# Performance work log

Hardware: AMD Instinct MI355X
Metric: run time of the kernel (lower is better)

The kernel has to match this reference:

```python
import jax, jax.numpy as jnp
import numpy as np

D_MODEL = 1024
NUM_HEADS = 16
DEPTH = D_MODEL // NUM_HEADS
B, S = 2, 2048
NEG = -1e9


def setup_inputs() -> dict:
    key = jax.random.key(0)
    ks = jax.random.split(key, 12)
    sc = 1.0 / np.sqrt(D_MODEL)
    inp = {
        "query": jax.random.normal(ks[0], (B, S, D_MODEL), jnp.float32),
        "key_in": jax.random.normal(ks[1], (B, S, D_MODEL), jnp.float32),
        "value": jax.random.normal(ks[2], (B, S, D_MODEL), jnp.float32),
        # causal mask: 1.0 where attention is disallowed (upper triangle)
        "mask": (1.0 - jnp.tril(jnp.ones((S, S), jnp.float32)))[None, None, :, :],
        "wq": jax.random.normal(ks[3], (D_MODEL, D_MODEL), jnp.float32) * sc,
        "bq": jnp.zeros((D_MODEL,), jnp.float32),
        "wk": jax.random.normal(ks[4], (D_MODEL, D_MODEL), jnp.float32) * sc,
        "bk": jnp.zeros((D_MODEL,), jnp.float32),
        "wv": jax.random.normal(ks[5], (D_MODEL, D_MODEL), jnp.float32) * sc,
        "bv": jnp.zeros((D_MODEL,), jnp.float32),
        "wo": jax.random.normal(ks[6], (D_MODEL, D_MODEL), jnp.float32) * sc,
        "bo": jnp.zeros((D_MODEL,), jnp.float32),
    }
    return inp


def _split_heads(x):
    # [B,S,D] -> [B,H,S,depth]
    b, s, _ = x.shape
    return x.reshape(b, s, NUM_HEADS, DEPTH).transpose(0, 2, 1, 3)


def reference(query, key_in, value, mask, wq, bq, wk, bk, wv, bv, wo, bo):
    q = _split_heads(query @ wq + bq)
    k = _split_heads(key_in @ wk + bk)
    v = _split_heads(value @ wv + bv)
    scale = 1.0 / jnp.sqrt(jnp.asarray(DEPTH, jnp.float32))
    logits = jnp.einsum("bhqd,bhkd->bhqk", q, k) * scale + mask * NEG
    attn = jax.nn.softmax(logits, axis=-1)
    out = jnp.einsum("bhqk,bhkd->bhqd", attn, v)  # [B,H,S,depth]
    out = out.transpose(0, 2, 1, 3).reshape(query.shape[0], -1, D_MODEL)
    return out @ wo + bo
```

## Files before the change

kernel.cpp:

```cpp
#include <hip/hip_runtime.h>
#include <hip/hip_bf16.h>
#include <cstdint>
#include <cstddef>

#define D_MODEL 1024
#define NHEADS  16
#define DEPTH   64
#define BATCH   2
#define SEQ     2048
#define M_TOT   (BATCH*SEQ)
#define QK_SCALE 0.18033688011112042f

typedef __attribute__((ext_vector_type(8)))  __bf16 bf16x8;
typedef __attribute__((ext_vector_type(4)))  float  f32x4;
typedef __attribute__((ext_vector_type(16))) float  f32x16;

__device__ inline unsigned short f2bf(float f){
  unsigned u = __float_as_uint(f);
  u += 0x7FFFu + ((u>>16)&1u);
  return (unsigned short)(u>>16);
}
__device__ inline unsigned cvtpk(float lo, float hi){
  unsigned r;
  asm("v_cvt_pk_bf16_f32 %0, %1, %2" : "=v"(r) : "v"(lo), "v"(hi));
  return r;
}
__device__ inline float fexp2(float x){
  float r;
  asm("v_exp_f32 %0, %1" : "=v"(r) : "v"(x));
  return r;
}
__device__ inline int bswap23(int x){
  return (x & ~12) | ((x & 4) << 1) | ((x & 8) >> 1);
}

#define AS1(p) ((__attribute__((address_space(1))) void*)(p))
#define AS3(p) ((__attribute__((address_space(3))) void*)(p))

__global__ void tcvt4(const float* __restrict__ w0, const float* __restrict__ w1,
                      const float* __restrict__ w2, const float* __restrict__ w3,
                      unsigned short* o0, unsigned short* o1,
                      unsigned short* o2, unsigned short* o3){
  const float* W = blockIdx.z==0 ? w0 : blockIdx.z==1 ? w1 : blockIdx.z==2 ? w2 : w3;
  unsigned short* Wt = blockIdx.z==0 ? o0 : blockIdx.z==1 ? o1 : blockIdx.z==2 ? o2 : o3;
  const bool perm = (blockIdx.z == 3);
  __shared__ float t[32][33];
  int bx = blockIdx.x*32, by = blockIdx.y*32;
  for (int j = threadIdx.y; j < 32; j += 8)
    t[j][threadIdx.x] = W[(size_t)(by+j)*D_MODEL + bx + threadIdx.x];
  __syncthreads();
  for (int j = threadIdx.y; j < 32; j += 8){
    int col = by + threadIdx.x;
    if (perm) col = bswap23(col);
    Wt[(size_t)(bx+j)*D_MODEL + col] = f2bf(t[threadIdx.x][j]);
  }
}

#define BK 32
#define GK 1024
#define NSTEP (GK/BK)

__global__ __launch_bounds__(256,4) void gemm_qkv(
    const float* __restrict__ Xfq, const float* __restrict__ Xfk,
    const float* __restrict__ Xfv,
    const unsigned short* __restrict__ Wq, const unsigned short* __restrict__ Wk,
    const unsigned short* __restrict__ Wv,
    const float* __restrict__ bq, const float* __restrict__ bk, const float* __restrict__ bv,
    unsigned short* Qh, unsigned short* Kh, unsigned short* Vth)
{
  __shared__ __align__(16) short As[2][64*BK];
  __shared__ __align__(16) short Bs[2][128*BK];
  const int z = blockIdx.z;
  const float* Af          = z==0 ? Xfq : z==1 ? Xfk : Xfv;
  const unsigned short* Bt = z==0 ? Wq  : z==1 ? Wk  : Wv;
  const float* bias        = z==0 ? bq  : z==1 ? bk  : bv;

  const int tid = threadIdx.x, lane = tid & 63, wave = tid >> 6;
  const int m0 = blockIdx.x*64, n0 = blockIdx.y*128;
  const int wm = wave >> 1, wn = wave & 1;

  f32x4 acc[2][4];
  #pragma unroll
  for (int i=0;i<2;i++)
    #pragma unroll
    for (int j=0;j<4;j++)
      acc[i][j] = (f32x4){0.f,0.f,0.f,0.f};

  const char* Afb   = (const char*)Af + (size_t)m0*GK*4;
  const char* Bbase = (const char*)Bt + (size_t)n0*GK*2;
  const int arow = tid >> 2;
  const int acb  = (tid & 3) * 32;

  float4 a0lo, a0hi, a1lo, a1hi;

#define LOADA0(k0) { \
    const char* p_ = Afb + (size_t)arow*(GK*4) + (size_t)(k0)*4 + acb; \
    a0lo = *(const float4*)p_; a0hi = *(const float4*)(p_ + 16); }
#define LOADA1(k0) { \
    const char* p_ = Afb + (size_t)arow*(GK*4) + (size_t)(k0)*4 + acb; \
    a1lo = *(const float4*)p_; a1hi = *(const float4*)(p_ + 16); }

#define ISSUEB(t, BUF) \
  _Pragma("unroll") \
  for (int c=0;c<2;c++) \
    __builtin_amdgcn_global_load_lds( \
      AS1(Bbase + (size_t)(c*64 + arow)*(GK*2) + (size_t)(t)*64 + (tid&3)*16), \
      AS3((char*)&Bs[BUF][0] + c*4096 + tid*16), 16, 0, 0);

#define CVTWR0() { \
    uint4 pk_; \
    pk_.x = cvtpk(a0lo.x, a0lo.y); pk_.y = cvtpk(a0lo.z, a0lo.w); \
    pk_.z = cvtpk(a0hi.x, a0hi.y); pk_.w = cvtpk(a0hi.z, a0hi.w); \
    *(uint4*)((char*)&As[0][0] + tid*16) = pk_; }
#define CVTWR1() { \
    uint4 pk_; \
    pk_.x = cvtpk(a1lo.x, a1lo.y); pk_.y = cvtpk(a1lo.z, a1lo.w); \
    pk_.z = cvtpk(a1hi.x, a1hi.y); pk_.w = cvtpk(a1hi.z, a1hi.w); \
    *(uint4*)((char*)&As[1][0] + tid*16) = pk_; }

#define MFMA_PHASE(BUF) { \
    bf16x8 af_[2], bv_[4]; \
    _Pragma("unroll") \
    for (int i=0;i<2;i++) \
      af_[i] = *(const bf16x8*)((const char*)&As[BUF][0] + (wm*32+i*16+(lane&15))*64 + (lane>>4)*16); \
    _Pragma("unroll") \
    for (int j=0;j<4;j++) \
      bv_[j] = *(const bf16x8*)((const char*)&Bs[BUF][0] + (wn*64+j*16+(lane&15))*64 + (lane>>4)*16); \
    _Pragma("unroll") \
    for (int i=0;i<2;i++) \
      _Pragma("unroll") \
      for (int j=0;j<4;j++) \
        acc[i][j] = __builtin_amdgcn_mfma_f32_16x16x32_bf16(af_[i], bv_[j], acc[i][j], 0,0,0); }

  LOADA0(0)
  ISSUEB(0, 0)
  LOADA1(BK)
  CVTWR0()

  #pragma unroll 1
  for (int t = 0; t < NSTEP; t += 2){
    __syncthreads();
    if (t+1 < NSTEP) ISSUEB(t+1, 1)
    if (t+2 < NSTEP) LOADA0((t+2)*BK)
    if (t+1 < NSTEP) CVTWR1()
    MFMA_PHASE(0)
    __syncthreads();
    if (t+2 < NSTEP) ISSUEB(t+2, 0)
    if (t+3 < NSTEP) LOADA1((t+3)*BK)
    if (t+2 < NSTEP) CVTWR0()
    MFMA_PHASE(1)
  }

  #pragma unroll
  for (int i=0;i<2;i++)
    #pragma unroll
    for (int j=0;j<4;j++)
      #pragma unroll
      for (int r=0;r<4;r++){
        int gr = m0 + wm*32 + i*16 + (lane>>4)*4 + r;
        int gc = n0 + wn*64 + j*16 + (lane&15);
        float v = acc[i][j][r] + bias[gc];
        int b = gr>>11, s = gr&2047, h = gc>>6, d = gc&63;
        if (z == 0){
          v *= QK_SCALE;
          Qh[(((size_t)(b*NHEADS+h))*SEQ + s)*DEPTH + d] = f2bf(v);
        } else if (z == 1){
          Kh[(((size_t)(b*NHEADS+h))*SEQ + s)*DEPTH + d] = f2bf(v);
        } else {
          int sp = bswap23(s);
          Vth[(((size_t)(b*NHEADS+h))*DEPTH + d)*SEQ + sp] = f2bf(v);
        }
      }
#undef LOADA0
#undef LOADA1
#undef ISSUEB
#undef CVTWR0
#undef CVTWR1
#undef MFMA_PHASE
}

__global__ __launch_bounds__(256,4) void gemm_out(
    const unsigned short* __restrict__ A,
    const unsigned short* __restrict__ Bt,
    const float* __restrict__ bias,
    float* __restrict__ Cout)
{
  __shared__ __align__(16) short As[2][64*BK];
  __shared__ __align__(16) short Bs[2][64*BK];
  const int tid = threadIdx.x, lane = tid & 63, wave = tid >> 6;
  const int m0 = blockIdx.x*64, n0 = blockIdx.y*64;
  const int wm = wave >> 1, wn = wave & 1;

  f32x4 acc[2][2];
  #pragma unroll
  for (int i=0;i<2;i++)
    #pragma unroll
    for (int j=0;j<2;j++)
      acc[i][j] = (f32x4){0.f,0.f,0.f,0.f};

  const char* Abase = (const char*)A + (size_t)m0*GK*2;
  const char* Bbase = (const char*)Bt + (size_t)n0*GK*2;

  auto STAGE = [&](int t){
    __builtin_amdgcn_global_load_lds(
      AS1(Abase + (size_t)(tid>>2)*(GK*2) + (size_t)t*64 + (tid&3)*16),
      AS3((char*)&As[t&1][0] + tid*16), 16, 0, 0);
    __builtin_amdgcn_global_load_lds(
      AS1(Bbase + (size_t)(tid>>2)*(GK*2) + (size_t)t*64 + (tid&3)*16),
      AS3((char*)&Bs[t&1][0] + tid*16), 16, 0, 0);
  };

  STAGE(0);
  #pragma unroll 1
  for (int t = 0; t < NSTEP; ++t){
    __syncthreads();
    if (t+1 < NSTEP) STAGE(t+1);
    bf16x8 af[2], bfv[2];
    #pragma unroll
    for (int i=0;i<2;i++)
      af[i] = *(const bf16x8*)((const char*)&As[t&1][0] + (wm*32 + i*16 + (lane&15))*64 + (lane>>4)*16);
    #pragma unroll
    for (int j=0;j<2;j++)
      bfv[j] = *(const bf16x8*)((const char*)&Bs[t&1][0] + (wn*32 + j*16 + (lane&15))*64 + (lane>>4)*16);
    #pragma unroll
    for (int i=0;i<2;i++)
      #pragma unroll
      for (int j=0;j<2;j++)
        acc[i][j] = __builtin_amdgcn_mfma_f32_16x16x32_bf16(af[i], bfv[j], acc[i][j], 0,0,0);
  }

  #pragma unroll
  for (int i=0;i<2;i++)
    #pragma unroll
    for (int j=0;j<2;j++)
      #pragma unroll
      for (int r=0;r<4;r++){
        int gr = m0 + wm*32 + i*16 + (lane>>4)*4 + r;
        int gc = n0 + wn*32 + j*16 + (lane&15);
        Cout[(size_t)gr*D_MODEL + gc] = acc[i][j][r] + bias[gc];
      }
}

__global__ __launch_bounds__(512,4) void attn_fwd(
  const unsigned short* __restrict__ Qh,
  const unsigned short* __restrict__ Kh,
  const unsigned short* __restrict__ Vt,
  unsigned short* __restrict__ AO)
{
  __shared__ __align__(16) short Ks[2][4096];
  __shared__ __align__(16) short Vs[2][4096];
  __shared__ float cbS[2][128];

  const int tid = threadIdx.x, lane = tid & 63, w = tid >> 6;
  const int h = lane >> 5, ql = lane & 31;
  const int qh = w & 1, kh = (w >> 1) & 1, tl = w >> 2;
  const int pj = blockIdx.x, bh = blockIdx.y;
  const size_t hb = (size_t)bh * SEQ * DEPTH;
  const char* Kb = (const char*)(Kh + hb);
  const char* Vb = (const char*)(Vt + hb);
  const unsigned short* Qb = Qh + hb;
  const int bb = bh >> 4, hd = bh & 15;
  const int swz = (ql & 7) << 4;

  auto STAGE = [&](int buf, int t){
    const int kv0 = t*64;
    #pragma unroll
    for (int i=0;i<2;i++){
      int c = (w&3)*2 + i;
      int x = c*1024 + lane*16;
      int row = x >> 7;
      int cb = (x & 127) ^ ((row&7)<<4);
      if (w < 4)
        __builtin_amdgcn_global_load_lds(
          AS1(Kb + (size_t)(kv0+row)*128 + cb),
          AS3((char*)&Ks[buf][0] + c*1024), 16, 0, 0);
      else
        __builtin_amdgcn_global_load_lds(
          AS1(Vb + ((size_t)row*SEQ + kv0)*2 + cb),
          AS3((char*)&Vs[buf][0] + c*1024), 16, 0, 0);
    }
  };

  const int jtw = tl ? pj : (31 - pj);
  const int Q0 = jtw*64 + qh*32;
  const int qmax = Q0 + 31;
  const int Tblock = 32 - pj;

  bf16x8 qreg[4];
  {
    const unsigned short* qp = Qb + (size_t)(Q0 + ql)*DEPTH + h*8;
    #pragma unroll
    for (int c=0;c<4;c++) qreg[c] = *(const bf16x8*)(qp + c*16);
  }

  f32x16 oacc[2];
  #pragma unroll
  for (int dh=0;dh<2;dh++)
    #pragma unroll
    for (int r=0;r<16;r++) oacc[dh][r] = 0.f;
  float s = 0.f;

  STAGE(0, 0);
  __syncthreads();
  int cur = 0;

  #pragma unroll 1
  for (int t = 0; t < Tblock; ++t){
    if (t+1 < Tblock) STAGE(cur^1, t+1);
    const int kvb = t*64 + kh*32;

    if (kvb <= qmax){
      f32x16 sa;
      #pragma unroll
      for (int r=0;r<16;r++) sa[r] = -16.0f;
      #pragma unroll
      for (int c=0;c<4;c++){
        bf16x8 kf = *(const bf16x8*)((const char*)&Ks[cur][0]
                      + (kh*32 + ql)*128 + ((32*c + 16*h) ^ swz));
        sa = __builtin_amdgcn_mfma_f32_32x32x16_bf16(kf, qreg[c], sa, 0,0,0);
      }

      if (kvb + 31 > Q0){
        const int qg = Q0 + ql - kvb;
        #pragma unroll
        for (int r=0;r<16;r++){
          int pos = (r&3) + 8*(r>>2) + 4*h;
          sa[r] = (pos > qg) ? -1e9f : sa[r];
        }
      }

      float s0=0.f, s1=0.f, s2=0.f, s3=0.f;
      #pragma unroll
      for (int r=0;r<16;r++){
        float p = fexp2(sa[r]);
        sa[r] = p;
        if ((r&3)==0) s0 += p; else if ((r&3)==1) s1 += p;
        else if ((r&3)==2) s2 += p; else s3 += p;
      }
      s += (s0+s1)+(s2+s3);

      bf16x8 pw[2];
      #pragma unroll
      for (int ks=0;ks<2;ks++){
        const int mm = 8*ks;
        union { unsigned u[4]; bf16x8 v; } pk;
        pk.u[0] = cvtpk(sa[mm+0], sa[mm+1]);
        pk.u[1] = cvtpk(sa[mm+2], sa[mm+3]);
        pk.u[2] = cvtpk(sa[mm+4], sa[mm+5]);
        pk.u[3] = cvtpk(sa[mm+6], sa[mm+7]);
        pw[ks] = pk.v;
      }

      #pragma unroll
      for (int ks=0;ks<2;ks++){
        #pragma unroll
        for (int dh=0;dh<2;dh++){
          bf16x8 vf = *(const bf16x8*)((const char*)&Vs[cur][0]
                        + (dh*32 + ql)*128 + ((kh*64 + ks*32 + 16*h) ^ swz));
          oacc[dh] = __builtin_amdgcn_mfma_f32_32x32x16_bf16(vf, pw[ks], oacc[dh], 0,0,0);
        }
      }
    }

    __syncthreads();
    cur ^= 1;
  }

  float* cbO  = (tl == 0) ? (float*)&Ks[0][0] : (float*)&Vs[0][0];
  float* cbSp = &cbS[tl][0];
  if (kh == 1){
    #pragma unroll
    for (int dh=0;dh<2;dh++)
      #pragma unroll
      for (int r=0;r<16;r++)
        cbO[(dh*16+r)*128 + qh*64 + lane] = oacc[dh][r];
    cbSp[qh*64 + lane] = s;
  }
  __syncthreads();
  if (kh == 0){
    #pragma unroll
    for (int dh=0;dh<2;dh++)
      #pragma unroll
      for (int r=0;r<16;r++)
        oacc[dh][r] += cbO[(dh*16+r)*128 + qh*64 + lane];
    s += cbSp[qh*64 + lane];
    float st = s + __shfl_xor(s, 32, 64);
    float inv = 1.0f / st;
    #pragma unroll
    for (int dh=0;dh<2;dh++)
      #pragma unroll
      for (int r=0;r<16;r++) oacc[dh][r] *= inv;

    unsigned short* orow = AO + ((size_t)bb*SEQ + (Q0 + ql))*D_MODEL + hd*DEPTH;
    #pragma unroll
    for (int dh=0;dh<2;dh++)
      #pragma unroll
      for (int g=0; g<2; g++){
        uint4 st4;
        st4.x = cvtpk(oacc[dh][8*g+0], oacc[dh][8*g+1]);
        st4.y = cvtpk(oacc[dh][8*g+2], oacc[dh][8*g+3]);
        st4.z = cvtpk(oacc[dh][8*g+4], oacc[dh][8*g+5]);
        st4.w = cvtpk(oacc[dh][8*g+6], oacc[dh][8*g+7]);
        *(uint4*)(orow + dh*32 + g*16 + h*8) = st4;
      }
  }
}

extern "C" void kernel_launch(void* const* d_in, const int* in_sizes, int n_in,
                              void* d_out, int out_size, void* d_ws, size_t ws_size,
                              hipStream_t stream) {
  const float* query  = (const float*)d_in[0];
  const float* key_in = (const float*)d_in[1];
  const float* value  = (const float*)d_in[2];
  const float* wq = (const float*)d_in[4];
  const float* bq = (const float*)d_in[5];
  const float* wk = (const float*)d_in[6];
  const float* bk = (const float*)d_in[7];
  const float* wv = (const float*)d_in[8];
  const float* bv = (const float*)d_in[9];
  const float* wo = (const float*)d_in[10];
  const float* bo = (const float*)d_in[11];

  char* ws = (char*)d_ws;
  const size_t MB = 1u<<20;
  unsigned short* Wtq = (unsigned short*)(ws + 24*MB);
  unsigned short* Wtk = (unsigned short*)(ws + 26*MB);
  unsigned short* Wtv = (unsigned short*)(ws + 28*MB);
  unsigned short* Wto = (unsigned short*)(ws + 30*MB);
  unsigned short* Qh  = (unsigned short*)(ws + 32*MB);
  unsigned short* Kh  = (unsigned short*)(ws + 40*MB);
  unsigned short* Vth = (unsigned short*)(ws + 48*MB);
  unsigned short* AO  = (unsigned short*)(ws + 56*MB);

  tcvt4<<<dim3(32,32,4), dim3(32,8), 0, stream>>>(wq, wk, wv, wo, Wtq, Wtk, Wtv, Wto);

  gemm_qkv<<<dim3(M_TOT/64, D_MODEL/128, 3), 256, 0, stream>>>(
      query, key_in, value, Wtq, Wtk, Wtv, bq, bk, bv, Qh, Kh, Vth);

  attn_fwd<<<dim3(16, BATCH*NHEADS), 512, 0, stream>>>(Qh, Kh, Vth, AO);

  gemm_out<<<dim3(M_TOT/64, D_MODEL/64), 256, 0, stream>>>(AO, Wto, bo, (float*)d_out);
}
```

Baseline: 121.4 us.

## Enlarge QKV GEMM tile to 128x128 and restructure its load/convert pipeline

The QKV projection GEMM now uses a 128x128 output tile per block instead of 64x128, so each B tile from LDS is reused across twice as many rows and the grid is halved. The main loop is reworked: the bf16 convert-and-store of A is moved after the MFMA phase, and __syncthreads is replaced by a custom barrier that waits only on partial vmcnt, with sched_barriers pinning instruction order. The aim is to cut global/LDS traffic per FLOP and overlap fp32 A loads with MFMA work. The cost is higher register and LDS use (launch bounds lowered to 3 waves per SIMD) and fewer blocks, which may reduce occupancy and latency hiding.

Result: faster. 110.2 us (-9.2%).

```diff
diff --git a/kernel.cpp b/kernel.cpp
--- a/kernel.cpp
+++ b/kernel.cpp
@@ -36,6 +36,13 @@
 
 #define AS1(p) ((__attribute__((address_space(1))) void*)(p))
 #define AS3(p) ((__attribute__((address_space(3))) void*)(p))
+#define SBAR() __builtin_amdgcn_sched_barrier(0)
+
+__device__ inline void bar_vm4_lg(){
+  asm volatile("s_waitcnt vmcnt(4) lgkmcnt(0)" ::: "memory");
+  __builtin_amdgcn_s_barrier();
+  __builtin_amdgcn_sched_barrier(0);
+}
 
 __global__ void tcvt4(const float* __restrict__ w0, const float* __restrict__ w1,
                       const float* __restrict__ w2, const float* __restrict__ w3,
@@ -60,7 +67,7 @@
 #define GK 1024
 #define NSTEP (GK/BK)
 
-__global__ __launch_bounds__(256,4) void gemm_qkv(
+__global__ __launch_bounds__(256,3) void gemm_qkv(
     const float* __restrict__ Xfq, const float* __restrict__ Xfk,
     const float* __restrict__ Xfv,
     const unsigned short* __restrict__ Wq, const unsigned short* __restrict__ Wk,
@@ -68,7 +75,7 @@
     const float* __restrict__ bq, const float* __restrict__ bk, const float* __restrict__ bv,
     unsigned short* Qh, unsigned short* Kh, unsigned short* Vth)
 {
-  __shared__ __align__(16) short As[2][64*BK];
+  __shared__ __align__(16) short As[2][128*BK];
   __shared__ __align__(16) short Bs[2][128*BK];
   const int z = blockIdx.z;
   const float* Af          = z==0 ? Xfq : z==1 ? Xfk : Xfv;
@@ -76,88 +83,103 @@
   const float* bias        = z==0 ? bq  : z==1 ? bk  : bv;
 
   const int tid = threadIdx.x, lane = tid & 63, wave = tid >> 6;
-  const int m0 = blockIdx.x*64, n0 = blockIdx.y*128;
+  const int m0 = blockIdx.x*128, n0 = blockIdx.y*128;
   const int wm = wave >> 1, wn = wave & 1;
 
-  f32x4 acc[2][4];
+  f32x4 acc[4][4];
   #pragma unroll
-  for (int i=0;i<2;i++)
+  for (int i=0;i<4;i++)
     #pragma unroll
     for (int j=0;j<4;j++)
       acc[i][j] = (f32x4){0.f,0.f,0.f,0.f};
 
   const char* Afb   = (const char*)Af + (size_t)m0*GK*4;
   const char* Bbase = (const char*)Bt + (size_t)n0*GK*2;
-  const int arow = tid >> 2;
-  const int acb  = (tid & 3) * 32;
-
-  float4 a0lo, a0hi, a1lo, a1hi;
-
-#define LOADA0(k0) { \
-    const char* p_ = Afb + (size_t)arow*(GK*4) + (size_t)(k0)*4 + acb; \
-    a0lo = *(const float4*)p_; a0hi = *(const float4*)(p_ + 16); }
-#define LOADA1(k0) { \
-    const char* p_ = Afb + (size_t)arow*(GK*4) + (size_t)(k0)*4 + acb; \
-    a1lo = *(const float4*)p_; a1hi = *(const float4*)(p_ + 16); }
-
-#define ISSUEB(t, BUF) \
+  const int arow = tid >> 1;
+  const int acf  = (tid & 1) * 64;
+  const int brow = tid >> 2;
+  const int bcb  = (tid & 3) * 16;
+
+  float4 s0_0, s0_1, s0_2, s0_3, s1_0, s1_1, s1_2, s1_3;
+
+#define LOADA_S0(k0) { \
+    const char* p_ = Afb + (size_t)arow*(GK*4) + (size_t)(k0)*4 + acf; \
+    s0_0 = *(const float4*)p_;        s0_1 = *(const float4*)(p_+16); \
+    s0_2 = *(const float4*)(p_+32);   s0_3 = *(const float4*)(p_+48); } \
+    SBAR();
+#define LOADA_S1(k0) { \
+    const char* p_ = Afb + (size_t)arow*(GK*4) + (size_t)(k0)*4 + acf; \
+    s1_0 = *(const float4*)p_;        s1_1 = *(const float4*)(p_+16); \
+    s1_2 = *(const float4*)(p_+32);   s1_3 = *(const float4*)(p_+48); } \
+    SBAR();
+
+#define ISSUEB(t, BUF) { \
   _Pragma("unroll") \
   for (int c=0;c<2;c++) \
     __builtin_amdgcn_global_load_lds( \
-      AS1(Bbase + (size_t)(c*64 + arow)*(GK*2) + (size_t)(t)*64 + (tid&3)*16), \
-      AS3((char*)&Bs[BUF][0] + c*4096 + tid*16), 16, 0, 0);
-
-#define CVTWR0() { \
-    uint4 pk_; \
-    pk_.x = cvtpk(a0lo.x, a0lo.y); pk_.y = cvtpk(a0lo.z, a0lo.w); \
-    pk_.z = cvtpk(a0hi.x, a0hi.y); pk_.w = cvtpk(a0hi.z, a0hi.w); \
-    *(uint4*)((char*)&As[0][0] + tid*16) = pk_; }
-#define CVTWR1() { \
-    uint4 pk_; \
-    pk_.x = cvtpk(a1lo.x, a1lo.y); pk_.y = cvtpk(a1lo.z, a1lo.w); \
-    pk_.z = cvtpk(a1hi.x, a1hi.y); pk_.w = cvtpk(a1hi.z, a1hi.w); \
-    *(uint4*)((char*)&As[1][0] + tid*16) = pk_; }
+      AS1(Bbase + (size_t)(c*64 + brow)*(GK*2) + (size_t)(t)*64 + bcb), \
+      AS3((char*)&Bs[BUF][0] + c*4096 + tid*16), 16, 0, 0); } \
+  SBAR();
+
+#define CVTWR_S0(BUF) { \
+    uint4 pka_, pkb_; \
+    pka_.x = cvtpk(s0_0.x, s0_0.y); pka_.y = cvtpk(s0_0.z, s0_0.w); \
+    pka_.z = cvtpk(s0_1.x, s0_1.y); pka_.w = cvtpk(s0_1.z, s0_1.w); \
+    pkb_.x = cvtpk(s0_2.x, s0_2.y); pkb_.y = cvtpk(s0_2.z, s0_2.w); \
+    pkb_.z = cvtpk(s0_3.x, s0_3.y); pkb_.w = cvtpk(s0_3.z, s0_3.w); \
+    *(uint4*)((char*)&As[BUF][0] + tid*32)      = pka_; \
+    *(uint4*)((char*)&As[BUF][0] + tid*32 + 16) = pkb_; }
+#define CVTWR_S1(BUF) { \
+    uint4 pka_, pkb_; \
+    pka_.x = cvtpk(s1_0.x, s1_0.y); pka_.y = cvtpk(s1_0.z, s1_0.w); \
+    pka_.z = cvtpk(s1_1.x, s1_1.y); pka_.w = cvtpk(s1_1.z, s1_1.w); \
+    pkb_.x = cvtpk(s1_2.x, s1_2.y); pkb_.y = cvtpk(s1_2.z, s1_2.w); \
+    pkb_.z = cvtpk(s1_3.x, s1_3.y); pkb_.w = cvtpk(s1_3.z, s1_3.w); \
+    *(uint4*)((char*)&As[BUF][0] + tid*32)      = pka_; \
+    *(uint4*)((char*)&As[BUF][0] + tid*32 + 16) = pkb_; }
 
 #define MFMA_PHASE(BUF) { \
-    bf16x8 af_[2], bv_[4]; \
+    bf16x8 af_[4], bv_[4]; \
     _Pragma("unroll") \
-    for (int i=0;i<2;i++) \
-      af_[i] = *(const bf16x8*)((const char*)&As[BUF][0] + (wm*32+i*16+(lane&15))*64 + (lane>>4)*16); \
+    for (int i=0;i<4;i++) \
+      af_[i] = *(const bf16x8*)((const char*)&As[BUF][0] + (wm*64+i*16+(lane&15))*64 + (lane>>4)*16); \
     _Pragma("unroll") \
     for (int j=0;j<4;j++) \
       bv_[j] = *(const bf16x8*)((const char*)&Bs[BUF][0] + (wn*64+j*16+(lane&15))*64 + (lane>>4)*16); \
     _Pragma("unroll") \
-    for (int i=0;i<2;i++) \
+    for (int i=0;i<4;i++) \
       _Pragma("unroll") \
       for (int j=0;j<4;j++) \
         acc[i][j] = __builtin_amdgcn_mfma_f32_16x16x32_bf16(af_[i], bv_[j], acc[i][j], 0,0,0); }
 
-  LOADA0(0)
   ISSUEB(0, 0)
-  LOADA1(BK)
-  CVTWR0()
+  LOADA_S0(0)
+  LOADA_S1(BK)
+  CVTWR_S0(0)
 
   #pragma unroll 1
   for (int t = 0; t < NSTEP; t += 2){
-    __syncthreads();
+    bar_vm4_lg();
     if (t+1 < NSTEP) ISSUEB(t+1, 1)
-    if (t+2 < NSTEP) LOADA0((t+2)*BK)
-    if (t+1 < NSTEP) CVTWR1()
+    if (t+2 < NSTEP) LOADA_S0((t+2)*BK)
     MFMA_PHASE(0)
-    __syncthreads();
-    if (t+2 < NSTEP) ISSUEB(t+2, 0)
-    if (t+3 < NSTEP) LOADA1((t+3)*BK)
-    if (t+2 < NSTEP) CVTWR0()
-    MFMA_PHASE(1)
+    if (t+1 < NSTEP) CVTWR_S1(1)
+    if (t+1 < NSTEP){
+      bar_vm4_lg();
+      if (t+2 < NSTEP) ISSUEB(t+2, 0)
+      if (t+3 < NSTEP) LOADA_S1((t+3)*BK)
+      MFMA_PHASE(1)
+      if (t+2 < NSTEP) CVTWR_S0(0)
+    }
   }
 
   #pragma unroll
-  for (int i=0;i<2;i++)
+  for (int i=0;i<4;i++)
     #pragma unroll
     for (int j=0;j<4;j++)
       #pragma unroll
       for (int r=0;r<4;r++){
-        int gr = m0 + wm*32 + i*16 + (lane>>4)*4 + r;
+        int gr = m0 + wm*64 + i*16 + (lane>>4)*4 + r;
         int gc = n0 + wn*64 + j*16 + (lane&15);
         float v = acc[i][j][r] + bias[gc];
         int b = gr>>11, s = gr&2047, h = gc>>6, d = gc&63;
@@ -171,11 +193,11 @@
           Vth[(((size_t)(b*NHEADS+h))*DEPTH + d)*SEQ + sp] = f2bf(v);
         }
       }
-#undef LOADA0
-#undef LOADA1
+#undef LOADA_S0
+#undef LOADA_S1
 #undef ISSUEB
-#undef CVTWR0
-#undef CVTWR1
+#undef CVTWR_S0
+#undef CVTWR_S1
 #undef MFMA_PHASE
 }
 
@@ -434,7 +456,7 @@
 
   tcvt4<<<dim3(32,32,4), dim3(32,8), 0, stream>>>(wq, wk, wv, wo, Wtq, Wtk, Wtv, Wto);
 
-  gemm_qkv<<<dim3(M_TOT/64, D_MODEL/128, 3), 256, 0, stream>>>(
+  gemm_qkv<<<dim3(M_TOT/128, D_MODEL/128, 3), 256, 0, stream>>>(
       query, key_in, value, Wtq, Wtk, Wtv, bq, bk, bv, Qh, Kh, Vth);
 
   attn_fwd<<<dim3(16, BATCH*NHEADS), 512, 0, stream>>>(Qh, Kh, Vth, AO);
```
